# Optimization experiments

Measured on AMD Instinct MI355X. Metric: run time of the kernel, lower is better.

The kernel has to match this reference:

```python
import jax, jax.numpy as jnp
import numpy as np

C, G, K, PAD = 64, 8, 9, 1  # channels, deformable groups, 3x3 taps, padding


def conv2d(x, w, b):
    y = jax.lax.conv_general_dilated(x, w, (1, 1), [(PAD, PAD), (PAD, PAD)],
                                     dimension_numbers=('NCHW', 'OIHW', 'NCHW'))
    return y + b[None, :, None, None]


def deform_conv(x, offset, w, b, groups):
    # x: [B,Cin,H,W]; offset: [B, 2*groups*K, H, W] laid out as (g, k, (dy,dx))
    B, Cin, H, W = x.shape
    Cg = Cin // groups
    dt = x.dtype
    off = offset.reshape(B, groups, K, 2, H, W)
    dy, dx = off[:, :, :, 0], off[:, :, :, 1]                  # [B,G,K,H,W]
    ky, kx = jnp.meshgrid(jnp.arange(3, dtype=dt), jnp.arange(3, dtype=dt), indexing='ij')
    ky, kx = ky.reshape(K), kx.reshape(K)
    grid_y = jnp.arange(H, dtype=dt)[None, None, None, :, None]
    grid_x = jnp.arange(W, dtype=dt)[None, None, None, None, :]
    py = grid_y - PAD + ky[None, None, :, None, None] + dy      # sample rows
    px = grid_x - PAD + kx[None, None, :, None, None] + dx      # sample cols

    y0 = jnp.floor(py)
    x0 = jnp.floor(px)
    xf = x.reshape(B, groups, Cg, H * W)

    def corner(yi, xi):
        valid = ((yi >= 0) & (yi <= H - 1) & (xi >= 0) & (xi <= W - 1)).astype(dt)
        idx = (jnp.clip(yi, 0, H - 1).astype(jnp.int32) * W
               + jnp.clip(xi, 0, W - 1).astype(jnp.int32)).reshape(B, groups, K * H * W)
        g = jax.vmap(jax.vmap(lambda f, i: f[:, i]))(xf, idx)   # [B,G,Cg,K*H*W]
        return g, valid.reshape(B, groups, 1, K * H * W)

    wy1 = (py - y0).reshape(B, groups, 1, -1)
    wx1 = (px - x0).reshape(B, groups, 1, -1)
    wy0, wx0 = 1.0 - wy1, 1.0 - wx1

    g00, v00 = corner(y0, x0)
    acc = g00 * (v00 * wy0 * wx0)
    g01, v01 = corner(y0, x0 + 1)
    acc = acc + g01 * (v01 * wy0 * wx1)
    g10, v10 = corner(y0 + 1, x0)
    acc = acc + g10 * (v10 * wy1 * wx0)
    g11, v11 = corner(y0 + 1, x0 + 1)
    acc = acc + g11 * (v11 * wy1 * wx1)

    sampled = acc.reshape(B, Cin, K, H, W)                      # G*Cg == Cin
    out = jnp.einsum('bckhw,ock->bohw', sampled, w.reshape(w.shape[0], Cin, K))
    return out + b[None, :, None, None]


def setup_inputs() -> dict:
    key = jax.random.key(0)
    ks = jax.random.split(key, 9)
    B, H, W = 2, 192, 192
    f = lambda k, s, sc=0.05: jax.random.normal(k, s, dtype=jnp.float32) * sc
    return dict(
        previous_features=jax.random.normal(ks[0], (B, C, H, W), dtype=jnp.float32),
        offsets=jax.random.normal(ks[1], (B, C, H, W), dtype=jnp.float32),
        w_off=f(ks[2], (2 * G * K, C, 3, 3), 0.01),
        b_off=jnp.zeros((2 * G * K,), jnp.float32),
        w_dcn=f(ks[3], (C, C, 3, 3)),
        b_dcn=f(ks[4], (C,)),
        w_r1=f(ks[5], (C, 2 * C, 3, 3)),
        b_r1=f(ks[6], (C,)),
        w_r2=f(ks[7], (C, C, 3, 3)),
        b_r2=f(ks[8], (C,)),
    )


def reference(previous_features, offsets, w_off, b_off, w_dcn, b_dcn, w_r1, b_r1, w_r2, b_r2):
    off = conv2d(offsets, w_off, b_off)                         # extra_offset_mask path
    aligned = deform_conv(previous_features, off, w_dcn, b_dcn, G)
    r = jnp.concatenate([aligned, previous_features], axis=1)
    r = jax.nn.leaky_relu(conv2d(r, w_r1, b_r1), 0.1)
    r = jax.nn.leaky_relu(conv2d(r, w_r2, b_r2), 0.1)
    return aligned + r
```

## Files before the change

### kernel.cpp

```cpp
#include <hip/hip_runtime.h>
#include <hip/hip_bf16.h>
#include <cstdint>
#include <cstddef>

constexpr int B_ = 2;
constexpr int HH = 192, WW = 192, HW_ = HH * WW;
constexpr int HP = 194, WPAD = 200;

typedef short bf16x8 __attribute__((ext_vector_type(8)));
typedef short s16x4  __attribute__((ext_vector_type(4)));
typedef float f32x4  __attribute__((ext_vector_type(4)));
typedef unsigned int u32x4 __attribute__((ext_vector_type(4)));

typedef __attribute__((address_space(1))) const void GLB;
typedef __attribute__((address_space(3))) void LDS;

__device__ __forceinline__ float bf2f(unsigned short h) {
  union { unsigned u; float f; } v; v.u = (unsigned)h << 16; return v.f;
}
__device__ __forceinline__ unsigned short f2bf(float f) {
  union { float f; unsigned u; } v; v.f = f;
  unsigned u = v.u;
  u += 0x7fffu + ((u >> 16) & 1u);
  return (unsigned short)(u >> 16);
}
__device__ __forceinline__ float leaky(float v) { return fmaxf(v, 0.1f * v); }

__global__ __launch_bounds__(256) void prep0(
    const float* __restrict__ offin,
    const float* __restrict__ w_off, const float* __restrict__ w_dcn,
    const float* __restrict__ w_r1,  const float* __restrict__ w_r2,
    unsigned short* __restrict__ offs_t, unsigned short* __restrict__ concat_t,
    unsigned short* __restrict__ r1_t,
    unsigned short* __restrict__ wOffB, unsigned short* __restrict__ wDcnB,
    unsigned short* __restrict__ wR1B,  unsigned short* __restrict__ wR2B)
{
  __shared__ float tile[16][65];
  int bid = blockIdx.x;
  int t = threadIdx.x;

  if (bid < 4608) {
    int bx = bid % 12, by = bid / 12;
    int xc = bx * 16;
    int y = by % HH, b = by / HH;
    #pragma unroll
    for (int cp = 0; cp < 4; ++cp) {
      int c = cp * 16 + (t >> 4);
      tile[t & 15][c] = offin[((size_t)(b * 64 + c) * HH + y) * WW + xc + (t & 15)];
    }
    __syncthreads();
    int x = t >> 4, c4 = (t & 15) * 4;
    s16x4 s;
    #pragma unroll
    for (int j = 0; j < 4; ++j) s[j] = (short)f2bf(tile[x][c4 + j]);
    *(s16x4*)&offs_t[((size_t)(b * HP + y + 1) * WPAD + xc + x + 1) * 64 + c4] = s;
  } else if (bid < 5508) {
    int tid = (bid - 4608) * 256 + t;
    const float* src; unsigned short* dst; int CI, CO, idx; bool dosw = true;
    if (tid < 82944)       { src = w_off; dst = wOffB; CI = 64;  CO = 144; idx = tid; }
    else if (tid < 119808) { src = w_dcn; dst = wDcnB; CI = 64;  CO = 64;  idx = tid - 82944; dosw = false; }
    else if (tid < 193536) { src = w_r1;  dst = wR1B;  CI = 128; CO = 64;  idx = tid - 119808; }
    else                   { src = w_r2;  dst = wR2B;  CI = 64;  CO = 64;  idx = tid - 193536; }
    int ci = idx % CI;
    int k  = (idx / CI) % 9;
    int o  = idx / (CI * 9);
    int pci = dosw ? (((((ci >> 3) ^ (o & 7))) << 3) | (ci & 7)) : ci;
    dst[((size_t)k * CO + o) * CI + pci] = f2bf(src[((size_t)o * CI + ci) * 9 + k]);
  } else {
    int tid = (bid - 5508) * 256 + t;
    if (tid >= B_ * HP * WPAD) return;
    int x = tid % WPAD, y = (tid / WPAD) % HP, b = tid / (HP * WPAD);
    bool border = (y == 0) || (y >= 193) || (x == 0) || (x >= 193);
    if (!border) return;
    size_t px = (size_t)(b * HP + y) * WPAD + x;
    u32x4 z4 = {0u, 0u, 0u, 0u};
    u32x4* p0 = (u32x4*)(offs_t   + px * 64);
    u32x4* p1 = (u32x4*)(concat_t + px * 128);
    u32x4* p2 = (u32x4*)(r1_t     + px * 64);
    #pragma unroll
    for (int i = 0; i < 8; ++i)  p0[i] = z4;
    #pragma unroll
    for (int i = 0; i < 16; ++i) p1[i] = z4;
    #pragma unroll
    for (int i = 0; i < 8; ++i)  p2[i] = z4;
  }
}

__global__ __launch_bounds__(256) void prep_prev(const float* __restrict__ src,
                                                 unsigned short* __restrict__ concatT,
                                                 unsigned short* __restrict__ gp)
{
  __shared__ float tile[16][65];
  int t = threadIdx.x;
  int xc = blockIdx.x * 16;
  int y = blockIdx.y % HH, b = blockIdx.y / HH;
  #pragma unroll
  for (int cp = 0; cp < 4; ++cp) {
    int c = cp * 16 + (t >> 4);
    tile[t & 15][c] = src[((size_t)(b * 64 + c) * HH + y) * WW + xc + (t & 15)];
  }
  __syncthreads();
  int x = t >> 4, c4 = (t & 15) * 4;
  s16x4 s;
  #pragma unroll
  for (int j = 0; j < 4; ++j) s[j] = (short)f2bf(tile[x][c4 + j]);
  *(s16x4*)&concatT[((size_t)(b * HP + y + 1) * WPAD + xc + x + 1) * 128 + 64 + c4] = s;
  int g = c4 >> 3, co = c4 & 7;
  *(s16x4*)&gp[((size_t)(b * 8 + g) * HW_ + (size_t)y * WW + xc + x) * 8 + co] = s;
}

template<int CIN, int COUT, int NF, bool LEAKY_, int OUTMODE, bool DBUF, bool REGPF>
__global__ __launch_bounds__(256, 4) void conv_mfma(
    const unsigned short* __restrict__ inT,
    const unsigned short* __restrict__ wS,
    const float* __restrict__ bias,
    const unsigned short* __restrict__ resid,
    void* __restrict__ outp)
{
  constexpr int CPP  = CIN / 8;
  constexpr int TPX  = 72;
  constexpr int NCH  = TPX * CPP;
  constexpr int RPR  = NCH / 64;
  constexpr int NREG = 3 * RPR;
  constexpr int WSZ  = NF * 16 * CIN;
  constexpr int WCH  = WSZ / 8;
  static_assert(WCH % 128 == 0, "staging must use full waves");
  static_assert(!REGPF || (WCH % 256 == 0), "REGPF needs whole chunks/thread");
  constexpr int RPT  = WCH / 256;
  __shared__ __align__(16) unsigned short tile[3 * TPX * CIN];
  __shared__ __align__(16) unsigned short wlds[(DBUF ? 2 : 1) * WSZ];

  const int t = threadIdx.x;
  const int l = t & 63, wv = t >> 6;
  const int lr = l & 15, lq = l >> 4, lk = lq * 8;

  constexpr int NWG = 3 * 384;
  int lin = blockIdx.x + 3 * blockIdx.y;
  int swz = (lin & 7) * (NWG / 8) + (lin >> 3);
  int xq = swz % 3, yy = swz / 3;
  int y = yy % HH, b = yy / HH;
  int x0 = xq * 64;
  const int co0 = blockIdx.z * (NF * 16);

  {
    const unsigned short* base = inT + ((size_t)(b * HP + y) * WPAD + x0) * CIN;
    for (int r = wv; r < NREG; r += 4) {
      int row = r / RPR;
      int rr  = r % RPR;
      int d   = rr * 64 + l;
      int p   = d / CPP;
      int cj  = d % CPP;
      int sc  = p * CPP + (cj ^ (p & (CPP - 1)));
      const unsigned short* src = base + (size_t)row * WPAD * CIN + (size_t)sc * 8;
      unsigned short* dst = &tile[(size_t)(row * NCH + rr * 64) * 8];
      __builtin_amdgcn_global_load_lds((GLB*)src, (LDS*)dst, 16, 0, 0);
    }
  }
  {
    const unsigned short* srcb = wS + (size_t)co0 * CIN;
    for (int r = t; r < WCH; r += 256)
      __builtin_amdgcn_global_load_lds((GLB*)(srcb + (size_t)r * 8),
                                       (LDS*)(&wlds[(size_t)r * 8]), 16, 0, 0);
  }
  __syncthreads();

  f32x4 acc[NF];
  #pragma unroll
  for (int f = 0; f < NF; ++f) acc[f] = f32x4{0.f, 0.f, 0.f, 0.f};

  #pragma unroll
  for (int k = 0; k < 9; ++k) {
    const int ky = k / 3, kx = k % 3;
    if (DBUF && k < 8) {
      const unsigned short* srcb = wS + (size_t)(k + 1) * COUT * CIN + (size_t)co0 * CIN;
      unsigned short* db = &wlds[(size_t)((k + 1) & 1) * WSZ];
      for (int r = t; r < WCH; r += 256)
        __builtin_amdgcn_global_load_lds((GLB*)(srcb + (size_t)r * 8),
                                         (LDS*)(db + (size_t)r * 8), 16, 0, 0);
    }
    u32x4 wpre[REGPF ? RPT : 1];
    if (REGPF && k < 8) {
      const unsigned short* srcb = wS + (size_t)(k + 1) * COUT * CIN + (size_t)co0 * CIN;
      #pragma unroll
      for (int r = 0; r < RPT; ++r)
        wpre[r] = *(const u32x4*)(srcb + (size_t)(t + r * 256) * 8);
    }
    {
      const unsigned short* wb = &wlds[DBUF ? (size_t)(k & 1) * WSZ : 0];
      const int px = wv * 16 + lr + kx;
      #pragma unroll
      for (int c = 0; c < CIN; c += 32) {
        int cj = (c + lk) >> 3;
        bf16x8 pf = *(const bf16x8*)
            &tile[(size_t)(ky * NCH + px * CPP + (cj ^ (px & (CPP - 1)))) * 8];
        #pragma unroll
        for (int f = 0; f < NF; ++f) {
          int co = f * 16 + lr;
          bf16x8 wf = *(const bf16x8*)&wb[(size_t)co * CIN + ((cj ^ (co & 7)) << 3)];
          if (OUTMODE == 0)
            acc[f] = __builtin_amdgcn_mfma_f32_16x16x32_bf16(pf, wf, acc[f], 0, 0, 0);
          else
            acc[f] = __builtin_amdgcn_mfma_f32_16x16x32_bf16(wf, pf, acc[f], 0, 0, 0);
        }
      }
    }
    if (DBUF) {
      __syncthreads();
    } else if (REGPF) {
      if (k < 8) {
        __syncthreads();
        #pragma unroll
        for (int r = 0; r < RPT; ++r)
          *(u32x4*)&wlds[(size_t)(t + r * 256) * 8] = wpre[r];
        __syncthreads();
      }
    } else if (k < 8) {
      __syncthreads();
      const unsigned short* srcb = wS + (size_t)(k + 1) * COUT * CIN + (size_t)co0 * CIN;
      for (int r = t; r < WCH; r += 256)
        __builtin_amdgcn_global_load_lds((GLB*)(srcb + (size_t)r * 8),
                                         (LDS*)(&wlds[(size_t)r * 8]), 16, 0, 0);
      __syncthreads();
    }
  }

  if (OUTMODE == 0) {
    int xs = x0 + wv * 16 + lq * 4;
    #pragma unroll
    for (int f = 0; f < NF; ++f) {
      int coG = co0 + f * 16 + lr;
      float bv = bias[coG];
      s16x4 s;
      #pragma unroll
      for (int j = 0; j < 4; ++j) {
        float v = acc[f][j] + bv;
        if (LEAKY_) v = leaky(v);
        s[j] = (short)f2bf(v);
      }
      *(s16x4*)((unsigned short*)outp + ((size_t)(b * COUT + coG) * HH + y) * WW + xs) = s;
    }
  } else if (OUTMODE == 1) {
    int x = x0 + wv * 16 + lr;
    #pragma unroll
    for (int f = 0; f < NF; ++f) {
      int coG = co0 + f * 16 + lq * 4;
      f32x4 bv = *(const f32x4*)&bias[coG];
      s16x4 s;
      #pragma unroll
      for (int j = 0; j < 4; ++j) {
        float v = acc[f][j] + bv[j];
        if (LEAKY_) v = leaky(v);
        s[j] = (short)f2bf(v);
      }
      *(s16x4*)((unsigned short*)outp + ((size_t)(b * HP + y + 1) * WPAD + x + 1) * 64 + coG) = s;
    }
  } else {
    int x = x0 + wv * 16 + lr;
    const unsigned short* rbase = resid + ((size_t)(b * HP + y + 1) * WPAD + x + 1) * 128;
    float* ob = (float*)outp + (size_t)b * 64 * HW_ + (size_t)y * WW + x;
    #pragma unroll
    for (int f = 0; f < NF; ++f) {
      int cobG = co0 + f * 16 + lq * 4;
      f32x4 bv = *(const f32x4*)&bias[cobG];
      s16x4 rv = *(const s16x4*)&rbase[cobG];
      #pragma unroll
      for (int j = 0; j < 4; ++j) {
        float v = acc[f][j] + bv[j];
        if (LEAKY_) v = leaky(v);
        v += bf2f((unsigned short)rv[j]);
        ob[(size_t)(cobG + j) * HW_] = v;
      }
    }
  }
}

__global__ __launch_bounds__(256, 4) void deform_mfma(
    const unsigned short* __restrict__ gp,
    const unsigned short* __restrict__ off,
    const unsigned short* __restrict__ wD,
    const float* __restrict__ bias,
    unsigned short* __restrict__ concatT)
{
  __shared__ __align__(16) unsigned short win[2048 * 8];
  const int t = threadIdx.x;
  const int l = t & 63, wv = t >> 6;
  const int lr = l & 15, lq = l >> 4;

  int lin = blockIdx.x;
  int swz = (lin & 7) * 144 + (lin >> 3);
  int xt = swz % 6;
  int rest = swz / 6;
  int yp = rest % 96, b = rest / 96;
  int Y = yp * 2, x0 = xt * 32;
  int yrow = Y + (wv >> 1);
  int xpix = x0 + (wv & 1) * 16 + lr;

  const int wy = Y - 2, wx = x0 - 3;
  const unsigned short* gpb = gp + (size_t)b * 8 * HW_ * 8;

  #pragma unroll
  for (int i = 0; i < 8; ++i) {
    int p  = t + i * 256;
    int g  = min(p / 241, 7);
    int rc = p - g * 241;
    int rcc = min(rc, 239);
    int r  = rcc / 40;
    int c  = rcc - r * 40;
    int yr = min(max(wy + r, 0), HH - 1);
    int xc = min(max(wx + c, 0), WW - 1);
    const unsigned short* src = gpb + ((size_t)g * HW_ + (size_t)yr * WW + xc) * 8;
    __builtin_amdgcn_global_load_lds((GLB*)src,
                                     (LDS*)(win + (size_t)p * 8), 16, 0, 0);
  }

  unsigned dd[2][9];
  #pragma unroll
  for (int gi = 0; gi < 2; ++gi) {
    int g = lq + gi * 4;
    const unsigned short* op = off + ((size_t)(b * 144 + g * 18) * HH + yrow) * WW + xpix;
    #pragma unroll
    for (int k = 0; k < 9; ++k) {
      unsigned dyv = op[(size_t)(2 * k) * HW_];
      unsigned dxv = op[(size_t)(2 * k + 1) * HW_];
      dd[gi][k] = dyv | (dxv << 16);
    }
  }

  __syncthreads();

  f32x4 acc[4];
  #pragma unroll
  for (int f = 0; f < 4; ++f) acc[f] = f32x4{0.f, 0.f, 0.f, 0.f};

  #pragma unroll
  for (int k = 0; k < 9; ++k) {
    const int ky = k / 3, kx = k % 3;
    bf16x8 pf0, pf1;
    #pragma unroll
    for (int gi = 0; gi < 2; ++gi) {
      int g = lq + gi * 4;
      float dyv = bf2f((unsigned short)(dd[gi][k] & 0xffffu));
      float dxv = bf2f((unsigned short)(dd[gi][k] >> 16));
      float py = (float)(yrow - 1 + ky) + dyv;
      float px = (float)(xpix - 1 + kx) + dxv;
      float fy0 = floorf(py), fx0 = floorf(px);
      float wy1 = py - fy0, wx1 = px - fx0;
      float wy0 = 1.f - wy1, wx0 = 1.f - wx1;
      bool vy0 = (fy0 >= 0.f)  && (fy0 <= 191.f);
      bool vy1 = (fy0 >= -1.f) && (fy0 <= 190.f);
      bool vx0 = (fx0 >= 0.f)  && (fx0 <= 191.f);
      bool vx1 = (fx0 >= -1.f) && (fx0 <= 190.f);
      float c00 = (vy0 && vx0) ? wy0 * wx0 : 0.f;
      float c01 = (vy0 && vx1) ? wy0 * wx1 : 0.f;
      float c10 = (vy1 && vx0) ? wy1 * wx0 : 0.f;
      float c11 = (vy1 && vx1) ? wy1 * wx1 : 0.f;
      int iy0 = (int)fminf(fmaxf(fy0, 0.f), 191.f);
      int iy1 = (int)fminf(fmaxf(fy0 + 1.f, 0.f), 191.f);
      int ix0 = (int)fminf(fmaxf(fx0, 0.f), 191.f);
      int ix1 = (int)fminf(fmaxf(fx0 + 1.f, 0.f), 191.f);
      bool inw = (iy0 >= wy) && (iy1 <= wy + 5) && (ix0 >= wx) && (ix1 <= wx + 39);
      int ry0 = min(max(iy0 - wy, 0), 5), ry1 = min(max(iy1 - wy, 0), 5);
      int rx0 = min(max(ix0 - wx, 0), 39), rx1 = min(max(ix1 - wx, 0), 39);
      const unsigned short* wg = win + (size_t)g * (241 * 8);
      bf16x8 v00 = *(const bf16x8*)(wg + ((size_t)ry0 * 40 + rx0) * 8);
      bf16x8 v01 = *(const bf16x8*)(wg + ((size_t)ry0 * 40 + rx1) * 8);
      bf16x8 v10 = *(const bf16x8*)(wg + ((size_t)ry1 * 40 + rx0) * 8);
      bf16x8 v11 = *(const bf16x8*)(wg + ((size_t)ry1 * 40 + rx1) * 8);
      if (!__all((int)inw)) {
        if (!inw) {
          const unsigned short* bb = gpb + (size_t)g * HW_ * 8;
          v00 = *(const bf16x8*)(bb + ((size_t)iy0 * WW + ix0) * 8);
          v01 = *(const bf16x8*)(bb + ((size_t)iy0 * WW + ix1) * 8);
          v10 = *(const bf16x8*)(bb + ((size_t)iy1 * WW + ix0) * 8);
          v11 = *(const bf16x8*)(bb + ((size_t)iy1 * WW + ix1) * 8);
        }
      }
      bf16x8 sv;
      #pragma unroll
      for (int j = 0; j < 8; ++j) {
        float s = bf2f((unsigned short)v00[j]) * c00
                + bf2f((unsigned short)v01[j]) * c01
                + bf2f((unsigned short)v10[j]) * c10
                + bf2f((unsigned short)v11[j]) * c11;
        sv[j] = (short)f2bf(s);
      }
      if (gi == 0) pf0 = sv; else pf1 = sv;
    }
    #pragma unroll
    for (int f = 0; f < 4; ++f) {
      bf16x8 wf = *(const bf16x8*)&wD[((size_t)k * 64 + f * 16 + lr) * 64 + lq * 8];
      acc[f] = __builtin_amdgcn_mfma_f32_16x16x32_bf16(wf, pf0, acc[f], 0, 0, 0);
    }
    #pragma unroll
    for (int f = 0; f < 4; ++f) {
      bf16x8 wf = *(const bf16x8*)&wD[((size_t)k * 64 + f * 16 + lr) * 64 + 32 + lq * 8];
      acc[f] = __builtin_amdgcn_mfma_f32_16x16x32_bf16(wf, pf1, acc[f], 0, 0, 0);
    }
  }

  unsigned short* outc = concatT + (size_t)b * HP * WPAD * 128;
  #pragma unroll
  for (int f = 0; f < 4; ++f) {
    int co = f * 16 + lq * 4;
    f32x4 bv = *(const f32x4*)&bias[co];
    s16x4 s;
    #pragma unroll
    for (int j = 0; j < 4; ++j) s[j] = (short)f2bf(acc[f][j] + bv[j]);
    *(s16x4*)&outc[((size_t)(yrow + 1) * WPAD + xpix + 1) * 128 + co] = s;
  }
}

extern "C" void kernel_launch(void* const* d_in, const int* in_sizes, int n_in,
                              void* d_out, int out_size, void* d_ws, size_t ws_size,
                              hipStream_t stream)
{
  const float* prev  = (const float*)d_in[0];
  const float* offin = (const float*)d_in[1];
  const float* w_off = (const float*)d_in[2];
  const float* b_off = (const float*)d_in[3];
  const float* w_dcn = (const float*)d_in[4];
  const float* b_dcn = (const float*)d_in[5];
  const float* w_r1  = (const float*)d_in[6];
  const float* b_r1  = (const float*)d_in[7];
  const float* w_r2  = (const float*)d_in[8];
  const float* b_r2  = (const float*)d_in[9];
  float* out = (float*)d_out;

  char* p = (char*)d_ws;
  unsigned short* offs_t   = (unsigned short*)p; p += (size_t)B_ * HP * WPAD * 64 * 2;
  unsigned short* concat_t = (unsigned short*)p; p += (size_t)B_ * HP * WPAD * 128 * 2;
  unsigned short* r1_t     = (unsigned short*)p; p += (size_t)B_ * HP * WPAD * 64 * 2;
  unsigned short* offf     = (unsigned short*)p; p += (size_t)B_ * 144 * HW_ * 2;
  unsigned short* wOffB    = (unsigned short*)p; p += 144 * 576 * 2;
  unsigned short* wDcnB    = (unsigned short*)p; p += 64 * 576 * 2;
  unsigned short* wR1B     = (unsigned short*)p; p += 64 * 1152 * 2;
  unsigned short* wR2B     = (unsigned short*)p; p += 64 * 576 * 2;
  unsigned short* gp = offs_t;

  prep0<<<5812, 256, 0, stream>>>(offin, w_off, w_dcn, w_r1, w_r2,
                                  offs_t, concat_t, r1_t,
                                  wOffB, wDcnB, wR1B, wR2B);

  conv_mfma<64, 144, 3, false, 0, true, false><<<dim3(3, 384, 3), 256, 0, stream>>>(
      offs_t, wOffB, b_off, nullptr, offf);

  prep_prev<<<dim3(12, 384), 256, 0, stream>>>(prev, concat_t, gp);

  deform_mfma<<<1152, 256, 0, stream>>>(gp, offf, wDcnB, b_dcn, concat_t);

  conv_mfma<128, 64, 4, true, 1, false, true><<<dim3(3, 384, 1), 256, 0, stream>>>(
      concat_t, wR1B, b_r1, nullptr, r1_t);

  conv_mfma<64, 64, 4, true, 2, true, false><<<dim3(3, 384, 1), 256, 0, stream>>>(
      r1_t, wR2B, b_r2, concat_t, out);
}
```

Measured before the change: 145.0 us.

## Fuse offset conv with prev-feature prep and move r1 border zeroing into conv kernel

Merges the offset-conv and the previous-feature transpose into one launch by putting the prep blocks on extra grid-z slices, so the memory-bound transpose can overlap with the MFMA conv. The gp buffer is moved from offs_t to r1_t so the prep no longer has to wait for the offset conv to finish reading offs_t. The r1_t border zeroing is moved from prep0 into the r1 conv launch. This removes a kernel launch and its drain gap. In exchange the fused kernel's LDS footprint is set by the larger conv body, which may limit occupancy of the prep blocks.

```diff
diff --git a/kernel.cpp b/kernel.cpp
--- a/kernel.cpp
+++ b/kernel.cpp
@@ -31,7 +31,6 @@
     const float* __restrict__ w_off, const float* __restrict__ w_dcn,
     const float* __restrict__ w_r1,  const float* __restrict__ w_r2,
     unsigned short* __restrict__ offs_t, unsigned short* __restrict__ concat_t,
-    unsigned short* __restrict__ r1_t,
     unsigned short* __restrict__ wOffB, unsigned short* __restrict__ wDcnB,
     unsigned short* __restrict__ wR1B,  unsigned short* __restrict__ wR2B)
 {
@@ -76,24 +75,19 @@
     u32x4 z4 = {0u, 0u, 0u, 0u};
     u32x4* p0 = (u32x4*)(offs_t   + px * 64);
     u32x4* p1 = (u32x4*)(concat_t + px * 128);
-    u32x4* p2 = (u32x4*)(r1_t     + px * 64);
     #pragma unroll
     for (int i = 0; i < 8; ++i)  p0[i] = z4;
     #pragma unroll
     for (int i = 0; i < 16; ++i) p1[i] = z4;
-    #pragma unroll
-    for (int i = 0; i < 8; ++i)  p2[i] = z4;
-  }
-}
-
-__global__ __launch_bounds__(256) void prep_prev(const float* __restrict__ src,
-                                                 unsigned short* __restrict__ concatT,
-                                                 unsigned short* __restrict__ gp)
-{
-  __shared__ float tile[16][65];
-  int t = threadIdx.x;
-  int xc = blockIdx.x * 16;
-  int y = blockIdx.y % HH, b = blockIdx.y / HH;
+  }
+}
+
+__device__ __forceinline__ void prep_prev_body(
+    const float* __restrict__ src, unsigned short* __restrict__ concatT,
+    unsigned short* __restrict__ gp, int bx, int by, float (*tile)[65], int t)
+{
+  int xc = bx * 16;
+  int y = by % HH, b = by / HH;
   #pragma unroll
   for (int cp = 0; cp < 4; ++cp) {
     int c = cp * 16 + (t >> 4);
@@ -110,12 +104,13 @@
 }
 
 template<int CIN, int COUT, int NF, bool LEAKY_, int OUTMODE, bool DBUF, bool REGPF>
-__global__ __launch_bounds__(256, 4) void conv_mfma(
+__device__ __forceinline__ void conv_body(
     const unsigned short* __restrict__ inT,
     const unsigned short* __restrict__ wS,
     const float* __restrict__ bias,
     const unsigned short* __restrict__ resid,
-    void* __restrict__ outp)
+    void* __restrict__ outp,
+    unsigned short* tile, unsigned short* wlds, int co0)
 {
   constexpr int CPP  = CIN / 8;
   constexpr int TPX  = 72;
@@ -127,8 +122,6 @@
   static_assert(WCH % 128 == 0, "staging must use full waves");
   static_assert(!REGPF || (WCH % 256 == 0), "REGPF needs whole chunks/thread");
   constexpr int RPT  = WCH / 256;
-  __shared__ __align__(16) unsigned short tile[3 * TPX * CIN];
-  __shared__ __align__(16) unsigned short wlds[(DBUF ? 2 : 1) * WSZ];
 
   const int t = threadIdx.x;
   const int l = t & 63, wv = t >> 6;
@@ -140,7 +133,6 @@
   int xq = swz % 3, yy = swz / 3;
   int y = yy % HH, b = yy / HH;
   int x0 = xq * 64;
-  const int co0 = blockIdx.z * (NF * 16);
 
   {
     const unsigned short* base = inT + ((size_t)(b * HP + y) * WPAD + x0) * CIN;
@@ -272,6 +264,65 @@
       }
     }
   }
+}
+
+__global__ __launch_bounds__(256, 4) void k1_fused(
+    const unsigned short* __restrict__ offs_t,
+    const unsigned short* __restrict__ wOffB,
+    const float* __restrict__ b_off,
+    unsigned short* __restrict__ offf,
+    const float* __restrict__ prev,
+    unsigned short* __restrict__ concat_t,
+    unsigned short* __restrict__ gp)
+{
+  __shared__ __align__(16) unsigned short tile[3 * 72 * 64];
+  __shared__ __align__(16) unsigned short wlds[2 * 3 * 16 * 64];
+  int z = blockIdx.z;
+  if (z < 3) {
+    conv_body<64, 144, 3, false, 0, true, false>(
+        offs_t, wOffB, b_off, nullptr, offf, tile, wlds, z * 48);
+  } else {
+    int pid = (z - 3) * 1152 + blockIdx.x + 3 * blockIdx.y;
+    prep_prev_body(prev, concat_t, gp, pid % 12, pid / 12,
+                   (float(*)[65])tile, threadIdx.x);
+  }
+}
+
+__global__ __launch_bounds__(256, 4) void conv_k3(
+    const unsigned short* __restrict__ concat_t,
+    const unsigned short* __restrict__ wR1B,
+    const float* __restrict__ b_r1,
+    unsigned short* __restrict__ r1_t)
+{
+  __shared__ __align__(16) unsigned short tile[3 * 72 * 128];
+  __shared__ __align__(16) unsigned short wlds[4 * 16 * 128];
+  if (blockIdx.z == 1) {
+    int tid = (blockIdx.x + 3 * blockIdx.y) * 256 + threadIdx.x;
+    if (tid >= B_ * HP * WPAD) return;
+    int x = tid % WPAD, y = (tid / WPAD) % HP, b = tid / (HP * WPAD);
+    bool border = (y == 0) || (y >= 193) || (x == 0) || (x >= 193);
+    if (!border) return;
+    u32x4 z4 = {0u, 0u, 0u, 0u};
+    u32x4* p2 = (u32x4*)(r1_t + ((size_t)(b * HP + y) * WPAD + x) * 64);
+    #pragma unroll
+    for (int i = 0; i < 8; ++i) p2[i] = z4;
+    return;
+  }
+  conv_body<128, 64, 4, true, 1, false, true>(
+      concat_t, wR1B, b_r1, nullptr, r1_t, tile, wlds, 0);
+}
+
+__global__ __launch_bounds__(256, 4) void conv_k4(
+    const unsigned short* __restrict__ r1_t,
+    const unsigned short* __restrict__ wR2B,
+    const float* __restrict__ b_r2,
+    const unsigned short* __restrict__ concat_t,
+    float* __restrict__ out)
+{
+  __shared__ __align__(16) unsigned short tile[3 * 72 * 64];
+  __shared__ __align__(16) unsigned short wlds[2 * 4 * 16 * 64];
+  conv_body<64, 64, 4, true, 2, true, false>(
+      r1_t, wR2B, b_r2, concat_t, out, tile, wlds, 0);
 }
 
 __global__ __launch_bounds__(256, 4) void deform_mfma(
@@ -435,22 +486,17 @@
   unsigned short* wDcnB    = (unsigned short*)p; p += 64 * 576 * 2;
   unsigned short* wR1B     = (unsigned short*)p; p += 64 * 1152 * 2;
   unsigned short* wR2B     = (unsigned short*)p; p += 64 * 576 * 2;
-  unsigned short* gp = offs_t;
+  unsigned short* gp = r1_t;
 
   prep0<<<5812, 256, 0, stream>>>(offin, w_off, w_dcn, w_r1, w_r2,
-                                  offs_t, concat_t, r1_t,
-                                  wOffB, wDcnB, wR1B, wR2B);
-
-  conv_mfma<64, 144, 3, false, 0, true, false><<<dim3(3, 384, 3), 256, 0, stream>>>(
-      offs_t, wOffB, b_off, nullptr, offf);
-
-  prep_prev<<<dim3(12, 384), 256, 0, stream>>>(prev, concat_t, gp);
+                                  offs_t, concat_t, wOffB, wDcnB, wR1B, wR2B);
+
+  k1_fused<<<dim3(3, 384, 7), 256, 0, stream>>>(
+      offs_t, wOffB, b_off, offf, prev, concat_t, gp);
 
   deform_mfma<<<1152, 256, 0, stream>>>(gp, offf, wDcnB, b_dcn, concat_t);
 
-  conv_mfma<128, 64, 4, true, 1, false, true><<<dim3(3, 384, 1), 256, 0, stream>>>(
-      concat_t, wR1B, b_r1, nullptr, r1_t);
-
-  conv_mfma<64, 64, 4, true, 2, true, false><<<dim3(3, 384, 1), 256, 0, stream>>>(
-      r1_t, wR2B, b_r2, concat_t, out);
-}
+  conv_k3<<<dim3(3, 384, 2), 256, 0, stream>>>(concat_t, wR1B, b_r1, r1_t);
+
+  conv_k4<<<dim3(3, 384, 1), 256, 0, stream>>>(r1_t, wR2B, b_r2, concat_t, out);
+}
```

Result: faster. 138.2 us (-4.7%).
